# Kernel tuning notes

Hardware: AMD Instinct MI355X
Metric: run time of the kernel (lower is better)

The kernel has to match this reference:

```python
import jax, jax.numpy as jnp
import numpy as np

# Dims from LiftSplatShootGPN defaults
B, N, D, FH, FW, C = 8, 6, 41, 8, 22, 64
OGFH, OGFW = 128, 352
DX = jnp.array([0.5, 0.5, 20.0], dtype=jnp.float32)        # gen_dx_bx
BX = jnp.array([-49.75, -49.75, 0.0], dtype=jnp.float32)
NX = (200, 200, 1)


def _frustum():
    # D x fH x fW x 3, matches create_frustum
    ds = jnp.broadcast_to(jnp.arange(4.0, 45.0, 1.0, dtype=jnp.float32).reshape(D, 1, 1), (D, FH, FW))
    xs = jnp.broadcast_to(jnp.linspace(0.0, OGFW - 1.0, FW, dtype=jnp.float32).reshape(1, 1, FW), (D, FH, FW))
    ys = jnp.broadcast_to(jnp.linspace(0.0, OGFH - 1.0, FH, dtype=jnp.float32).reshape(1, FH, 1), (D, FH, FW))
    return jnp.stack((xs, ys, ds), -1)


def setup_inputs() -> dict:
    key = jax.random.key(0)
    k1, k2, k3, k4, k5, k6 = jax.random.split(key, 6)
    eye = jnp.eye(3, dtype=jnp.float32)
    x_feats = jax.random.normal(k1, (B, N, D, FH, FW, C), dtype=jnp.float32)
    # well-conditioned camera extrinsics / intrinsics
    rots = eye + 0.1 * jax.random.normal(k2, (B, N, 3, 3), dtype=jnp.float32)
    trans = 2.0 * jax.random.normal(k3, (B, N, 3), dtype=jnp.float32)
    intr_base = jnp.array([[278.0, 0.0, 176.0], [0.0, 278.0, 64.0], [0.0, 0.0, 1.0]], dtype=jnp.float32)
    intrins = intr_base + 0.5 * jax.random.normal(k4, (B, N, 3, 3), dtype=jnp.float32) * jnp.array([[1, 0, 1], [0, 1, 1], [0, 0, 0]], dtype=jnp.float32)
    post_rots = eye + 0.01 * jax.random.normal(k5, (B, N, 3, 3), dtype=jnp.float32)
    post_trans = 0.5 * jax.random.normal(k6, (B, N, 3), dtype=jnp.float32)
    return {"x_feats": x_feats, "rots": rots, "trans": trans, "intrins": intrins,
            "post_rots": post_rots, "post_trans": post_trans}


def _forward(x_feats, rots, trans, intrins, post_rots, post_trans):
    frustum = _frustum()  # [D,FH,FW,3]
    # get_geometry: undo image-space augmentation
    pts = frustum[None, None] - post_trans[:, :, None, None, None, :]            # [B,N,D,H,W,3]
    inv_pr = jnp.linalg.inv(post_rots)                                           # [B,N,3,3]
    pts = jnp.einsum('bnij,bndhwj->bndhwi', inv_pr, pts)
    # unproject: (u*d, v*d, d)
    pts = jnp.concatenate((pts[..., :2] * pts[..., 2:3], pts[..., 2:3]), axis=-1)
    combine = jnp.einsum('bnij,bnjk->bnik', rots, jnp.linalg.inv(intrins))
    geom = jnp.einsum('bnij,bndhwj->bndhwi', combine, pts) + trans[:, :, None, None, None, :]

    # voxel_pooling
    Nprime = B * N * D * FH * FW
    x = x_feats.reshape(Nprime, C)
    # torch .long() truncates toward zero -> astype(int32) matches
    g = ((geom - (BX - DX / 2.0)) / DX).reshape(Nprime, 3).astype(jnp.int32)
    bix = jnp.repeat(jnp.arange(B, dtype=jnp.int32), Nprime // B)
    kept = ((g[:, 0] >= 0) & (g[:, 0] < NX[0]) &
            (g[:, 1] >= 0) & (g[:, 1] < NX[1]) &
            (g[:, 2] >= 0) & (g[:, 2] < NX[2]))
    # QuickCumsum computes per-voxel segment sums; scatter-add of all kept points
    # into the dense grid yields identical values without the sort.
    flat = ((bix * NX[2] + g[:, 2]) * NX[0] + g[:, 0]) * NX[1] + g[:, 1]
    flat = jnp.where(kept, flat, 0)
    xm = jnp.where(kept[:, None], x, jnp.zeros((), x.dtype))
    grid = jnp.zeros((B * NX[2] * NX[0] * NX[1], C), dtype=x.dtype).at[flat].add(xm)
    # final: [B, C, nz, nx0, nx1] -> cat over nz (nz=1) -> [B, C, 200, 200]
    grid = grid.reshape(B, NX[2], NX[0], NX[1], C)
    final = jnp.transpose(grid, (0, 1, 4, 2, 3)).reshape(B, NX[2] * C, NX[0], NX[1])
    return final


def reference(x_feats, rots, trans, intrins, post_rots, post_trans):
    return _forward(x_feats, rots, trans, intrins, post_rots, post_trans)
```

## Files before the change

kernel.cpp:

```cpp
#include <hip/hip_runtime.h>

#define B_   8
#define N_   6
#define D_   41
#define FH_  8
#define FW_  22
#define C_   64
#define NPRIME (B_*N_*D_*FH_*FW_)
#define NBLK_PTS 1353
#define NX0  200
#define NX1  200
#define G1Q  4
#define NB2  (B_ * NX0 * G1Q)
#define OUTSZ (B_*C_*NX0*NX1)
#define MAXTASKS 16384
#define GATHER_BLOCKS 1024
#define CLS0 384
#define CLS1 96

__device__ void lapack_inv3_f32(const float Ain[9], float Aout[9]) {
    #pragma clang fp contract(off)
    float a[9];
    for (int r = 0; r < 3; ++r)
        for (int c = 0; c < 3; ++c)
            a[c*3 + r] = Ain[r*3 + c];
    int ipiv[3];
    for (int j = 0; j < 3; ++j) {
        int p = j;
        float amax = fabsf(a[j*3 + j]);
        for (int i = j + 1; i < 3; ++i) {
            float v = fabsf(a[j*3 + i]);
            if (v > amax) { amax = v; p = i; }
        }
        ipiv[j] = p;
        if (p != j)
            for (int c = 0; c < 3; ++c) { float t = a[c*3+j]; a[c*3+j] = a[c*3+p]; a[c*3+p] = t; }
        float d = 1.0f / a[j*3 + j];
        for (int i = j + 1; i < 3; ++i) a[j*3 + i] = a[j*3 + i] * d;
        for (int jj = j + 1; jj < 3; ++jj) {
            float temp = -a[jj*3 + j];
            for (int ii = j + 1; ii < 3; ++ii)
                a[jj*3 + ii] = a[jj*3 + ii] + a[j*3 + ii] * temp;
        }
    }
    for (int j = 0; j < 3; ++j) {
        float ajj_inv = 1.0f / a[j*3 + j];
        a[j*3 + j] = ajj_inv;
        float AJJ = -ajj_inv;
        for (int jj = 0; jj < j; ++jj) {
            float temp = a[j*3 + jj];
            for (int i = 0; i < jj; ++i)
                a[j*3 + i] = a[j*3 + i] + temp * a[jj*3 + i];
            a[j*3 + jj] = a[j*3 + jj] * a[jj*3 + jj];
        }
        for (int i = 0; i < j; ++i) a[j*3 + i] = a[j*3 + i] * AJJ;
    }
    float work[3];
    for (int j = 2; j >= 0; --j) {
        for (int i = j + 1; i < 3; ++i) { work[i] = a[j*3 + i]; a[j*3 + i] = 0.0f; }
        for (int jj = j + 1; jj < 3; ++jj) {
            float temp = -work[jj];
            for (int i = 0; i < 3; ++i)
                a[j*3 + i] = a[j*3 + i] + temp * a[jj*3 + i];
        }
    }
    for (int j = 2; j >= 0; --j) {
        int p = ipiv[j];
        if (p != j)
            for (int i = 0; i < 3; ++i) { float t = a[j*3+i]; a[j*3+i] = a[p*3+i]; a[p*3+i] = t; }
    }
    for (int r = 0; r < 3; ++r)
        for (int c = 0; c < 3; ++c)
            Aout[r*3 + c] = a[c*3 + r];
}

__global__ void prep_kernel(const float* __restrict__ rots,
                            const float* __restrict__ trans,
                            const float* __restrict__ intrins,
                            const float* __restrict__ post_rots,
                            const float* __restrict__ post_trans,
                            float* __restrict__ mats,
                            int* __restrict__ counts) {
    #pragma clang fp contract(off)
    int t = threadIdx.x;
    for (int i = t; i < NB2; i += 256) counts[i] = 0;
    if (t >= B_ * N_) return;
    float pr[9], ipr[9], K[9], iK[9];
    for (int i = 0; i < 9; ++i) { pr[i] = post_rots[t*9 + i]; K[i] = intrins[t*9 + i]; }
    lapack_inv3_f32(pr, ipr);
    lapack_inv3_f32(K, iK);
    float* m = mats + t * 24;
    for (int i = 0; i < 9; ++i) m[i] = ipr[i];
    for (int i = 0; i < 3; ++i)
        for (int k = 0; k < 3; ++k) {
            float s = rots[t*9 + i*3 + 0] * iK[0*3 + k];
            s = s + rots[t*9 + i*3 + 1] * iK[1*3 + k];
            s = s + rots[t*9 + i*3 + 2] * iK[2*3 + k];
            m[9 + i*3 + k] = s;
        }
    for (int i = 0; i < 3; ++i) {
        m[18 + i] = post_trans[t*3 + i];
        m[21 + i] = trans[t*3 + i];
    }
}

__global__ void __launch_bounds__(256) geom_kernel(
        const float* __restrict__ mats,
        unsigned int* __restrict__ pcode,
        int* __restrict__ counts) {
    #pragma clang fp contract(off)
    __shared__ unsigned int hist[NB2];
    int t = threadIdx.x;
    int p = blockIdx.x * 256 + t;
    for (int i = t; i < NB2; i += 256) hist[i] = 0u;
    __syncthreads();

    int w  = p % FW_;
    int h  = (p / FW_) % FH_;
    int d  = (p / (FW_ * FH_)) % D_;
    int bn = p / (FW_ * FH_ * D_);
    int b  = bn / N_;

    const float* m = mats + bn * 24;

    float xs = (w == FW_ - 1) ? 351.0f : (float)((double)w * (351.0 / 21.0));
    float ys = (h == FH_ - 1) ? 127.0f : (float)((double)h * (127.0 / 7.0));
    float ds = 4.0f + (float)d;

    float px = xs - m[18], py = ys - m[19], pz = ds - m[20];
    float qx = m[0]*px;  qx = qx + m[1]*py;  qx = qx + m[2]*pz;
    float qy = m[3]*px;  qy = qy + m[4]*py;  qy = qy + m[5]*pz;
    float qz = m[6]*px;  qz = qz + m[7]*py;  qz = qz + m[8]*pz;

    float ux = qx * qz, uy = qy * qz, uz = qz;

    float gx = m[9]*ux;   gx = gx + m[10]*uy;  gx = gx + m[11]*uz;  gx = gx + m[21];
    float gy = m[12]*ux;  gy = gy + m[13]*uy;  gy = gy + m[14]*uz;  gy = gy + m[22];
    float gz = m[15]*ux;  gz = gz + m[16]*uy;  gz = gz + m[17]*uz;  gz = gz + m[23];

    float cx = (gx - (-50.0f)) / 0.5f;
    float cy = (gy - (-50.0f)) / 0.5f;
    float cz = (gz - (-10.0f)) / 20.0f;
    int g0 = (int)cx;
    int g1 = (int)cy;
    int g2 = (int)cz;

    bool kept = (g0 >= 0) && (g0 < NX0) && (g1 >= 0) && (g1 < NX1) && (g2 == 0);
    if (kept) {
        int g1q = g1 / 50;
        int g1r = g1 - g1q * 50;
        int bk  = (b * NX0 + g0) * G1Q + g1q;
        pcode[p] = ((unsigned int)bk << 6) | (unsigned int)g1r;
        atomicAdd(&hist[bk], 1u);
    } else {
        pcode[p] = 0xFFFFFFFFu;
    }
    __syncthreads();
    for (int i = t; i < NB2; i += 256) {
        unsigned int hv = hist[i];
        if (hv) atomicAdd(&counts[i], (int)hv);
    }
}

__global__ void scan_kernel(const int* __restrict__ counts,
                            int* __restrict__ offsets,
                            int* __restrict__ cursor,
                            unsigned int* __restrict__ tasks,
                            int* __restrict__ task_count) {
    __shared__ int ts[256];
    __shared__ int s0[256], s1[256], s2[256], s3[256];
    int t = threadIdx.x;
    const int PER = NB2 / 256;
    int base = t * PER;
    int mysum = 0;
    int c0 = 0, c1 = 0, c2 = 0, c3 = 0;
    for (int j = 0; j < PER; ++j) {
        int c = counts[base + j];
        mysum += c;
        if (c >= CLS0) c0++;
        else if (c >= CLS1) c1++;
        else if (c > 0) c2++;
        else c3++;
    }
    ts[t] = mysum; s0[t] = c0; s1[t] = c1; s2[t] = c2; s3[t] = c3;
    __syncthreads();
    for (int off = 1; off < 256; off <<= 1) {
        int v  = (t >= off) ? ts[t - off] : 0;
        int a0 = (t >= off) ? s0[t - off] : 0;
        int a1 = (t >= off) ? s1[t - off] : 0;
        int a2 = (t >= off) ? s2[t - off] : 0;
        int a3 = (t >= off) ? s3[t - off] : 0;
        __syncthreads();
        ts[t] += v; s0[t] += a0; s1[t] += a1; s2[t] += a2; s3[t] += a3;
        __syncthreads();
    }
    int run = (t > 0) ? ts[t - 1] : 0;
    int tot0 = s0[255], tot1 = s1[255], tot2 = s2[255];
    int p0 = ((t > 0) ? s0[t - 1] : 0);
    int p1 = tot0 + ((t > 0) ? s1[t - 1] : 0);
    int p2 = tot0 + tot1 + ((t > 0) ? s2[t - 1] : 0);
    int p3 = tot0 + tot1 + tot2 + ((t > 0) ? s3[t - 1] : 0);
    for (int j = 0; j < PER; ++j) {
        int c = counts[base + j];
        offsets[base + j] = run;
        cursor[base + j]  = run;
        run += c;
        unsigned int bkid = (unsigned int)(base + j);
        if (c >= CLS0)      tasks[p0++] = bkid;
        else if (c >= CLS1) tasks[p1++] = bkid;
        else if (c > 0)     tasks[p2++] = bkid;
        else                tasks[p3++] = bkid;
    }
    if (t == 255) {
        offsets[NB2] = run;
        task_count[0] = NB2;
    }
}

__global__ void __launch_bounds__(256) place_kernel(
        const unsigned int* __restrict__ pcode,
        int* __restrict__ cursor,
        unsigned int* __restrict__ entries) {
    __shared__ int cnt[NB2];
    int t = threadIdx.x;
    int p = blockIdx.x * 256 + t;
    for (int i = t; i < NB2; i += 256) cnt[i] = 0;
    __syncthreads();
    unsigned int code = pcode[p];
    bool kept = (code != 0xFFFFFFFFu);
    int bk = (int)(code >> 6);
    int lr = 0;
    if (kept) lr = atomicAdd(&cnt[bk], 1);
    __syncthreads();
    for (int i = t; i < NB2; i += 256) {
        int c = cnt[i];
        if (c) cnt[i] = atomicAdd(&cursor[i], c);
    }
    __syncthreads();
    if (kept)
        entries[cnt[bk] + lr] = ((code & 63u) << 19) | (unsigned int)p;
}

#define LDS_STRIDE 51
__global__ void __launch_bounds__(512) gather_kernel(
        const float* __restrict__ x_feats,
        const unsigned int* __restrict__ entries,
        const int* __restrict__ offsets,
        const unsigned int* __restrict__ tasks,
        float* __restrict__ out) {
    __shared__ float acc[C_ * LDS_STRIDE];
    int t = threadIdx.x, wave = t >> 6, lane = t & 63;

    for (int tid = blockIdx.x; tid < NB2; tid += GATHER_BLOCKS) {
        int bk = (int)tasks[tid];
        int s = offsets[bk];
        int e = offsets[bk + 1];
        int n = e - s;

        int b   = bk / (NX0 * G1Q);
        int rem = bk % (NX0 * G1Q);
        int g0  = rem / G1Q, g1q = rem % G1Q;
        size_t obase = (size_t)b * (C_ * NX0 * NX1) + (size_t)g0 * NX1 + g1q * 50;

        if (n == 0) {
            float2 z2 = make_float2(0.f, 0.f);
            for (int k = t; k < C_ * 25; k += 512) {
                int c = k / 25, r2 = k - c * 25;
                *(float2*)&out[obase + (size_t)c * (NX0 * NX1) + (size_t)(r2 * 2)] = z2;
            }
            continue;
        }

        for (int i = t; i < C_ * LDS_STRIDE; i += 512) acc[i] = 0.0f;
        __syncthreads();

        int nfull = (n >> 6) << 6;
        for (int sbase = 0; sbase < nfull; sbase += 64) {
            int i0 = s + sbase + wave * 8;
            unsigned int v0 = entries[i0],     v1 = entries[i0 + 1];
            unsigned int v2 = entries[i0 + 2], v3 = entries[i0 + 3];
            unsigned int v4 = entries[i0 + 4], v5 = entries[i0 + 5];
            unsigned int v6 = entries[i0 + 6], v7 = entries[i0 + 7];
            float f0 = x_feats[(size_t)(v0 & 0x7FFFFu) * C_ + lane];
            float f1 = x_feats[(size_t)(v1 & 0x7FFFFu) * C_ + lane];
            float f2 = x_feats[(size_t)(v2 & 0x7FFFFu) * C_ + lane];
            float f3 = x_feats[(size_t)(v3 & 0x7FFFFu) * C_ + lane];
            float f4 = x_feats[(size_t)(v4 & 0x7FFFFu) * C_ + lane];
            float f5 = x_feats[(size_t)(v5 & 0x7FFFFu) * C_ + lane];
            float f6 = x_feats[(size_t)(v6 & 0x7FFFFu) * C_ + lane];
            float f7 = x_feats[(size_t)(v7 & 0x7FFFFu) * C_ + lane];
            int lb = lane * LDS_STRIDE;
            atomicAdd(&acc[lb + (int)(v0 >> 19)], f0);
            atomicAdd(&acc[lb + (int)(v1 >> 19)], f1);
            atomicAdd(&acc[lb + (int)(v2 >> 19)], f2);
            atomicAdd(&acc[lb + (int)(v3 >> 19)], f3);
            atomicAdd(&acc[lb + (int)(v4 >> 19)], f4);
            atomicAdd(&acc[lb + (int)(v5 >> 19)], f5);
            atomicAdd(&acc[lb + (int)(v6 >> 19)], f6);
            atomicAdd(&acc[lb + (int)(v7 >> 19)], f7);
        }
        for (int i = nfull + wave; i < n; i += 8) {
            unsigned int v = entries[s + i];
            float f = x_feats[(size_t)(v & 0x7FFFFu) * C_ + lane];
            atomicAdd(&acc[lane * LDS_STRIDE + (int)(v >> 19)], f);
        }
        __syncthreads();

        for (int k = t; k < C_ * 25; k += 512) {
            int c = k / 25, r2 = k - c * 25;
            float2 v = make_float2(acc[c * LDS_STRIDE + 2 * r2],
                                   acc[c * LDS_STRIDE + 2 * r2 + 1]);
            *(float2*)&out[obase + (size_t)c * (NX0 * NX1) + (size_t)(r2 * 2)] = v;
        }
        __syncthreads();
    }
}

extern "C" void kernel_launch(void* const* d_in, const int* in_sizes, int n_in,
                              void* d_out, int out_size, void* d_ws, size_t ws_size,
                              hipStream_t stream) {
    const float* x_feats    = (const float*)d_in[0];
    const float* rots       = (const float*)d_in[1];
    const float* trans      = (const float*)d_in[2];
    const float* intrins    = (const float*)d_in[3];
    const float* post_rots  = (const float*)d_in[4];
    const float* post_trans = (const float*)d_in[5];
    float* out = (float*)d_out;

    char* w = (char*)d_ws;
    float*        mats       = (float*)w;         w += 48 * 24 * sizeof(float);
    int*          counts     = (int*)w;           w += NB2 * sizeof(int);
    int*          offsets    = (int*)w;           w += (NB2 + 1) * sizeof(int);
    int*          cursor     = (int*)w;           w += NB2 * sizeof(int);
    int*          task_count = (int*)w;           w += 4 * sizeof(int);
    unsigned int* tasks      = (unsigned int*)w;  w += MAXTASKS * sizeof(unsigned int);
    unsigned int* pcode      = (unsigned int*)w;  w += NPRIME * sizeof(unsigned int);
    unsigned int* entries    = (unsigned int*)w;  w += NPRIME * sizeof(unsigned int);

    prep_kernel<<<1, 256, 0, stream>>>(rots, trans, intrins, post_rots, post_trans,
                                       mats, counts);
    geom_kernel<<<NBLK_PTS, 256, 0, stream>>>(mats, pcode, counts);
    scan_kernel<<<1, 256, 0, stream>>>(counts, offsets, cursor, tasks, task_count);
    place_kernel<<<NBLK_PTS, 256, 0, stream>>>(pcode, cursor, entries);
    gather_kernel<<<GATHER_BLOCKS, 512, 0, stream>>>(x_feats, entries, offsets,
                                                     tasks, out);
}
```

Baseline: 212.9 us.

## Replace per-bucket gather with channel-pair row-band render kernel

Replaces the per-bucket gather, which gave each block one row-quarter across all 64 channels, with a render kernel. Each of B*32 blocks owns two channels of one batch and walks the grid in 16-row bands, accumulating into LDS and writing contiguous float4 rows of the output planes. Buckets become row halves, the task-class sorting in the scan is dropped, and entries now carry the local row and full column. The cost is that every point entry is re-read by 32 blocks, once per channel pair, each loading only 8 bytes of features. The aim is to trade scattered per-bucket work and small strided output writes for coalesced plane writes.

```diff
diff --git a/kernel.cpp b/kernel.cpp
--- a/kernel.cpp
+++ b/kernel.cpp
@@ -8,15 +8,13 @@
 #define C_   64
 #define NPRIME (B_*N_*D_*FH_*FW_)
 #define NBLK_PTS 1353
+#define PTS_PER_CAM (D_*FH_*FW_)
 #define NX0  200
 #define NX1  200
-#define G1Q  4
-#define NB2  (B_ * NX0 * G1Q)
+#define G1H  2
+#define NB2  (B_ * NX0 * G1H)
 #define OUTSZ (B_*C_*NX0*NX1)
-#define MAXTASKS 16384
-#define GATHER_BLOCKS 1024
-#define CLS0 384
-#define CLS1 96
+#define RROWS 16
 
 __device__ void lapack_inv3_f32(const float Ain[9], float Aout[9]) {
     #pragma clang fp contract(off)
@@ -118,7 +116,7 @@
     int w  = p % FW_;
     int h  = (p / FW_) % FH_;
     int d  = (p / (FW_ * FH_)) % D_;
-    int bn = p / (FW_ * FH_ * D_);
+    int bn = p / PTS_PER_CAM;
     int b  = bn / N_;
 
     const float* m = mats + bn * 24;
@@ -147,10 +145,10 @@
 
     bool kept = (g0 >= 0) && (g0 < NX0) && (g1 >= 0) && (g1 < NX1) && (g2 == 0);
     if (kept) {
-        int g1q = g1 / 50;
-        int g1r = g1 - g1q * 50;
-        int bk  = (b * NX0 + g0) * G1Q + g1q;
-        pcode[p] = ((unsigned int)bk << 6) | (unsigned int)g1r;
+        int g1h = g1 / 100;
+        int r   = g1 - g1h * 100;
+        int bk  = (b * NX0 + g0) * G1H + g1h;
+        pcode[p] = ((unsigned int)bk << 7) | (unsigned int)r;
         atomicAdd(&hist[bk], 1u);
     } else {
         pcode[p] = 0xFFFFFFFFu;
@@ -164,57 +162,28 @@
 
 __global__ void scan_kernel(const int* __restrict__ counts,
                             int* __restrict__ offsets,
-                            int* __restrict__ cursor,
-                            unsigned int* __restrict__ tasks,
-                            int* __restrict__ task_count) {
-    __shared__ int ts[256];
-    __shared__ int s0[256], s1[256], s2[256], s3[256];
-    int t = threadIdx.x;
-    const int PER = NB2 / 256;
+                            int* __restrict__ cursor) {
+    __shared__ int ts[128];
+    int t = threadIdx.x;
+    const int PER = NB2 / 128;
     int base = t * PER;
     int mysum = 0;
-    int c0 = 0, c1 = 0, c2 = 0, c3 = 0;
+    for (int j = 0; j < PER; ++j) mysum += counts[base + j];
+    ts[t] = mysum;
+    __syncthreads();
+    for (int off = 1; off < 128; off <<= 1) {
+        int v = (t >= off) ? ts[t - off] : 0;
+        __syncthreads();
+        ts[t] += v;
+        __syncthreads();
+    }
+    int run = (t > 0) ? ts[t - 1] : 0;
     for (int j = 0; j < PER; ++j) {
-        int c = counts[base + j];
-        mysum += c;
-        if (c >= CLS0) c0++;
-        else if (c >= CLS1) c1++;
-        else if (c > 0) c2++;
-        else c3++;
-    }
-    ts[t] = mysum; s0[t] = c0; s1[t] = c1; s2[t] = c2; s3[t] = c3;
-    __syncthreads();
-    for (int off = 1; off < 256; off <<= 1) {
-        int v  = (t >= off) ? ts[t - off] : 0;
-        int a0 = (t >= off) ? s0[t - off] : 0;
-        int a1 = (t >= off) ? s1[t - off] : 0;
-        int a2 = (t >= off) ? s2[t - off] : 0;
-        int a3 = (t >= off) ? s3[t - off] : 0;
-        __syncthreads();
-        ts[t] += v; s0[t] += a0; s1[t] += a1; s2[t] += a2; s3[t] += a3;
-        __syncthreads();
-    }
-    int run = (t > 0) ? ts[t - 1] : 0;
-    int tot0 = s0[255], tot1 = s1[255], tot2 = s2[255];
-    int p0 = ((t > 0) ? s0[t - 1] : 0);
-    int p1 = tot0 + ((t > 0) ? s1[t - 1] : 0);
-    int p2 = tot0 + tot1 + ((t > 0) ? s2[t - 1] : 0);
-    int p3 = tot0 + tot1 + tot2 + ((t > 0) ? s3[t - 1] : 0);
-    for (int j = 0; j < PER; ++j) {
-        int c = counts[base + j];
         offsets[base + j] = run;
         cursor[base + j]  = run;
-        run += c;
-        unsigned int bkid = (unsigned int)(base + j);
-        if (c >= CLS0)      tasks[p0++] = bkid;
-        else if (c >= CLS1) tasks[p1++] = bkid;
-        else if (c > 0)     tasks[p2++] = bkid;
-        else                tasks[p3++] = bkid;
-    }
-    if (t == 255) {
-        offsets[NB2] = run;
-        task_count[0] = NB2;
-    }
+        run += counts[base + j];
+    }
+    if (t == 127) offsets[NB2] = run;
 }
 
 __global__ void __launch_bounds__(256) place_kernel(
@@ -228,7 +197,7 @@
     __syncthreads();
     unsigned int code = pcode[p];
     bool kept = (code != 0xFFFFFFFFu);
-    int bk = (int)(code >> 6);
+    int bk = (int)(code >> 7);
     int lr = 0;
     if (kept) lr = atomicAdd(&cnt[bk], 1);
     __syncthreads();
@@ -237,80 +206,60 @@
         if (c) cnt[i] = atomicAdd(&cursor[i], c);
     }
     __syncthreads();
-    if (kept)
-        entries[cnt[bk] + lr] = ((code & 63u) << 19) | (unsigned int)p;
-}
-
-#define LDS_STRIDE 51
-__global__ void __launch_bounds__(512) gather_kernel(
+    if (kept) {
+        int r   = (int)(code & 127u);
+        int bh  = bk >> 1;
+        int g0  = bh % NX0;
+        int g1  = (bk & 1) * 100 + r;
+        entries[cnt[bk] + lr] = ((unsigned int)(g0 & 15) << 27) |
+                                ((unsigned int)g1 << 19) | (unsigned int)p;
+    }
+}
+
+__global__ void __launch_bounds__(1024) render_kernel(
         const float* __restrict__ x_feats,
         const unsigned int* __restrict__ entries,
         const int* __restrict__ offsets,
-        const unsigned int* __restrict__ tasks,
         float* __restrict__ out) {
-    __shared__ float acc[C_ * LDS_STRIDE];
-    int t = threadIdx.x, wave = t >> 6, lane = t & 63;
-
-    for (int tid = blockIdx.x; tid < NB2; tid += GATHER_BLOCKS) {
-        int bk = (int)tasks[tid];
-        int s = offsets[bk];
-        int e = offsets[bk + 1];
-        int n = e - s;
-
-        int b   = bk / (NX0 * G1Q);
-        int rem = bk % (NX0 * G1Q);
-        int g0  = rem / G1Q, g1q = rem % G1Q;
-        size_t obase = (size_t)b * (C_ * NX0 * NX1) + (size_t)g0 * NX1 + g1q * 50;
-
-        if (n == 0) {
-            float2 z2 = make_float2(0.f, 0.f);
-            for (int k = t; k < C_ * 25; k += 512) {
-                int c = k / 25, r2 = k - c * 25;
-                *(float2*)&out[obase + (size_t)c * (NX0 * NX1) + (size_t)(r2 * 2)] = z2;
-            }
-            continue;
-        }
-
-        for (int i = t; i < C_ * LDS_STRIDE; i += 512) acc[i] = 0.0f;
-        __syncthreads();
-
-        int nfull = (n >> 6) << 6;
-        for (int sbase = 0; sbase < nfull; sbase += 64) {
-            int i0 = s + sbase + wave * 8;
-            unsigned int v0 = entries[i0],     v1 = entries[i0 + 1];
-            unsigned int v2 = entries[i0 + 2], v3 = entries[i0 + 3];
-            unsigned int v4 = entries[i0 + 4], v5 = entries[i0 + 5];
-            unsigned int v6 = entries[i0 + 6], v7 = entries[i0 + 7];
-            float f0 = x_feats[(size_t)(v0 & 0x7FFFFu) * C_ + lane];
-            float f1 = x_feats[(size_t)(v1 & 0x7FFFFu) * C_ + lane];
-            float f2 = x_feats[(size_t)(v2 & 0x7FFFFu) * C_ + lane];
-            float f3 = x_feats[(size_t)(v3 & 0x7FFFFu) * C_ + lane];
-            float f4 = x_feats[(size_t)(v4 & 0x7FFFFu) * C_ + lane];
-            float f5 = x_feats[(size_t)(v5 & 0x7FFFFu) * C_ + lane];
-            float f6 = x_feats[(size_t)(v6 & 0x7FFFFu) * C_ + lane];
-            float f7 = x_feats[(size_t)(v7 & 0x7FFFFu) * C_ + lane];
-            int lb = lane * LDS_STRIDE;
-            atomicAdd(&acc[lb + (int)(v0 >> 19)], f0);
-            atomicAdd(&acc[lb + (int)(v1 >> 19)], f1);
-            atomicAdd(&acc[lb + (int)(v2 >> 19)], f2);
-            atomicAdd(&acc[lb + (int)(v3 >> 19)], f3);
-            atomicAdd(&acc[lb + (int)(v4 >> 19)], f4);
-            atomicAdd(&acc[lb + (int)(v5 >> 19)], f5);
-            atomicAdd(&acc[lb + (int)(v6 >> 19)], f6);
-            atomicAdd(&acc[lb + (int)(v7 >> 19)], f7);
-        }
-        for (int i = nfull + wave; i < n; i += 8) {
-            unsigned int v = entries[s + i];
-            float f = x_feats[(size_t)(v & 0x7FFFFu) * C_ + lane];
-            atomicAdd(&acc[lane * LDS_STRIDE + (int)(v >> 19)], f);
-        }
-        __syncthreads();
-
-        for (int k = t; k < C_ * 25; k += 512) {
-            int c = k / 25, r2 = k - c * 25;
-            float2 v = make_float2(acc[c * LDS_STRIDE + 2 * r2],
-                                   acc[c * LDS_STRIDE + 2 * r2 + 1]);
-            *(float2*)&out[obase + (size_t)c * (NX0 * NX1) + (size_t)(r2 * 2)] = v;
+    __shared__ float acc[2 * RROWS * NX1];
+    const int CHS = RROWS * NX1;
+    int blk = blockIdx.x;
+    int b  = blk >> 5;
+    int cp = blk & 31;
+    int c0 = cp * 2;
+    int t = threadIdx.x;
+    size_t pl0 = ((size_t)b * C_ + c0) * (NX0 * NX1);
+    size_t pl1 = pl0 + (size_t)(NX0 * NX1);
+
+    for (int g = 0; g < (NX0 + RROWS - 1) / RROWS; ++g) {
+        int row0  = g * RROWS;
+        int nrows = (NX0 - row0 < RROWS) ? (NX0 - row0) : RROWS;
+        int nf    = nrows * NX1;
+
+        for (int i = t; i < 2 * CHS; i += 1024) acc[i] = 0.0f;
+        __syncthreads();
+
+        int bk0 = b * (NX0 * G1H) + row0 * G1H;
+        int s = offsets[bk0];
+        int e = offsets[bk0 + nrows * G1H];
+        for (int i = s + t; i < e; i += 1024) {
+            unsigned int v = entries[i];
+            int p  = (int)(v & 0x7FFFFu);
+            int g1 = (int)((v >> 19) & 0xFFu);
+            int rl = (int)(v >> 27);
+            float2 f = *(const float2*)&x_feats[(size_t)p * C_ + c0];
+            int a = rl * NX1 + g1;
+            atomicAdd(&acc[a], f.x);
+            atomicAdd(&acc[CHS + a], f.y);
+        }
+        __syncthreads();
+
+        int nf4 = nf >> 2;
+        size_t ob = (size_t)row0 * NX1;
+        for (int k = t; k < 2 * nf4; k += 1024) {
+            int ch = k / nf4, kk = k - ch * nf4;
+            float4 v = *(float4*)&acc[ch * CHS + kk * 4];
+            *(float4*)&out[(ch ? pl1 : pl0) + ob + (size_t)kk * 4] = v;
         }
         __syncthreads();
     }
@@ -332,16 +281,13 @@
     int*          counts     = (int*)w;           w += NB2 * sizeof(int);
     int*          offsets    = (int*)w;           w += (NB2 + 1) * sizeof(int);
     int*          cursor     = (int*)w;           w += NB2 * sizeof(int);
-    int*          task_count = (int*)w;           w += 4 * sizeof(int);
-    unsigned int* tasks      = (unsigned int*)w;  w += MAXTASKS * sizeof(unsigned int);
     unsigned int* pcode      = (unsigned int*)w;  w += NPRIME * sizeof(unsigned int);
     unsigned int* entries    = (unsigned int*)w;  w += NPRIME * sizeof(unsigned int);
 
     prep_kernel<<<1, 256, 0, stream>>>(rots, trans, intrins, post_rots, post_trans,
                                        mats, counts);
     geom_kernel<<<NBLK_PTS, 256, 0, stream>>>(mats, pcode, counts);
-    scan_kernel<<<1, 256, 0, stream>>>(counts, offsets, cursor, tasks, task_count);
+    scan_kernel<<<1, 128, 0, stream>>>(counts, offsets, cursor);
     place_kernel<<<NBLK_PTS, 256, 0, stream>>>(pcode, cursor, entries);
-    gather_kernel<<<GATHER_BLOCKS, 512, 0, stream>>>(x_feats, entries, offsets,
-                                                     tasks, out);
-}
+    render_kernel<<<B_ * 32, 1024, 0, stream>>>(x_feats, entries, offsets, out);
+}
```

New measurement: 191.9 us. -9.9%, faster.
